# Performance work log

Measured on AMD Instinct MI355X. Metric: run time of the kernel, lower is better.

Reference implementation:

```python
import jax, jax.numpy as jnp
import numpy as np

BS = 32  # leaf block size


def setup_inputs() -> dict:
    key = jax.random.key(0)
    ks = jax.random.split(key, 10)
    N, C, E, H = 262144, 128, 4194304, 4
    x = jax.random.normal(ks[0], (1, N, C), jnp.float32)
    rows = jax.random.randint(ks[1], (E,), 0, N, dtype=jnp.int32)
    offs = jax.random.randint(ks[2], (E,), -16, 16, dtype=jnp.int32)
    cols = jnp.clip(rows + offs, 0, N - 1)
    edge_index = jnp.stack([rows, cols], axis=0)  # (2, E) int32
    edge_values = jax.random.normal(ks[3], (E,), jnp.float32)
    positions = jax.random.uniform(ks[4], (N, 3), jnp.float32)
    qkv_w = jax.random.normal(ks[5], (C, 3 * C), jnp.float32) * 0.02
    qkv_b = jnp.zeros((3 * C,), jnp.float32)
    proj_w = jax.random.normal(ks[6], (C, C), jnp.float32) * 0.02
    proj_b = jnp.zeros((C,), jnp.float32)
    gate_w = jax.random.normal(ks[7], (H, 1), jnp.float32) * 0.01  # nn.Linear(1, H)
    gate_b = jnp.zeros((H,), jnp.float32)
    return {"x": x, "edge_index": edge_index, "edge_values": edge_values,
            "positions": positions, "qkv_w": qkv_w, "qkv_b": qkv_b,
            "proj_w": proj_w, "proj_b": proj_b, "gate_w": gate_w, "gate_b": gate_b}


def _build_leaf_block_connectivity(edge_index, edge_values, positions, num_blocks, dtype):
    # Returns attn_mask (nb, 32, 33) and edge_feats (nb, 32, 33, 4) = (dx,dy,dz,w).
    rows, cols = edge_index[0], edge_index[1]
    br, bc = rows // BS, cols // BS
    in_blk = (br == bc) & (br < num_blocks)
    b_safe = jnp.where(in_blk, br, num_blocks)  # out-of-block edges -> dummy block
    rl, cl = rows % BS, cols % BS
    dx = positions[cols] - positions[rows]               # (E, 3)
    ef_flat = jnp.concatenate([dx, edge_values[:, None]], axis=1).astype(dtype)  # (E, 4)
    diag = jnp.arange(BS)
    attn_mask = jnp.zeros((num_blocks + 1, BS, BS + 1), dtype)
    attn_mask = attn_mask.at[:, diag, diag].set(1.0)      # self
    attn_mask = attn_mask.at[:, :, BS].set(1.0)           # block node
    attn_mask = attn_mask.at[b_safe, rl, cl].set(1.0)     # edges
    edge_feats = jnp.zeros((num_blocks + 1, BS, BS + 1, 4), dtype)
    edge_feats = edge_feats.at[b_safe, rl, cl].set(ef_flat)
    return attn_mask[:num_blocks], edge_feats[:num_blocks]


def reference(x, edge_index, edge_values, positions, qkv_w, qkv_b, proj_w, proj_b, gate_w, gate_b):
    B, N, C = x.shape
    H = gate_b.shape[0]
    hd = C // H
    scale = hd ** -0.5
    nb = N // BS
    dtype = x.dtype
    attn_mask, edge_feats = _build_leaf_block_connectivity(edge_index, edge_values, positions, nb, dtype)

    x_blk = x.reshape(B, nb, BS, C)
    block_node = x_blk.mean(axis=2, keepdims=True)            # (B, nb, 1, C)
    kv = jnp.concatenate([x_blk, block_node], axis=2)          # (B, nb, 33, C)
    qkv_q = x_blk @ qkv_w + qkv_b
    qkv_kv = kv @ qkv_w + qkv_b
    q = qkv_q[..., :C].reshape(B, nb, BS, H, hd)
    k = qkv_kv[..., C:2 * C].reshape(B, nb, BS + 1, H, hd)
    v = qkv_kv[..., 2 * C:].reshape(B, nb, BS + 1, H, hd)

    scores = jnp.einsum('bnqhd,bnkhd->bnqkh', q, k) * scale    # (B, nb, 32, 33, H)

    diag = jnp.arange(BS)
    w_bias = edge_feats[..., 3]                                # (nb, 32, 33)
    w_bias = w_bias.at[:, :, BS].set(1.0)
    w_bias = w_bias.at[:, diag, diag].set(1.0)
    scores = scores + w_bias[None, :, :, :, None]

    mask = attn_mask[None, :, :, :, None]                      # (1, nb, 32, 33, 1)
    neg = jnp.asarray(-1e9, dtype)
    scores = jnp.where(mask == 0, neg, scores)
    attn_probs = jax.nn.softmax(scores, axis=3)

    # edge_gate: Linear(1, H) applied to w_bias, zeroed where masked, added post-softmax
    gate = w_bias[..., None] * gate_w[:, 0] + gate_b           # (nb, 32, 33, H)
    gate = jnp.where(mask[0] == 0, 0.0, gate)[None]            # (1, nb, 32, 33, H)
    combined = attn_probs + gate

    out = jnp.einsum('bnqkh,bnkhd->bnqhd', combined, v).reshape(B, N, C)
    return out @ proj_w + proj_b
```

## Files before the change

### kernel.cpp

```cpp
#include <hip/hip_runtime.h>
#include <hip/hip_bf16.h>

#define BS 32
#define NBC 33

typedef unsigned long long ull;
typedef __attribute__((ext_vector_type(8))) __bf16 bf16x8;
typedef __attribute__((ext_vector_type(4))) float f32x4;

__device__ __forceinline__ unsigned short f2b(float f) {
    __hip_bfloat16 h = __float2bfloat16(f);
    return *reinterpret_cast<unsigned short*>(&h);
}
__device__ __forceinline__ float b2f(unsigned short u) {
    union { unsigned int i; float f; } x; x.i = ((unsigned int)u) << 16; return x.f;
}
#define LD8(p) (*reinterpret_cast<const bf16x8*>(p))

__global__ void zero_kernel(uint4* __restrict__ p, int n4) {
    int stride = gridDim.x * blockDim.x;
    for (int i = blockIdx.x * blockDim.x + threadIdx.x; i < n4; i += stride)
        p[i] = make_uint4(0u, 0u, 0u, 0u);
}

__global__ void edge_scatter_kernel(const int* __restrict__ rows,
                                    const int* __restrict__ cols,
                                    unsigned* __restrict__ tbl, int E) {
    int base = (blockIdx.x * 256 + threadIdx.x) * 4;
    if (base >= E) return;
    if (base + 4 <= E) {
        int4 r4 = *reinterpret_cast<const int4*>(rows + base);
        int4 c4 = *reinterpret_cast<const int4*>(cols + base);
        int rr[4] = {r4.x, r4.y, r4.z, r4.w};
        int cc[4] = {c4.x, c4.y, c4.z, c4.w};
        #pragma unroll
        for (int k = 0; k < 4; ++k) {
            int r = rr[k], c = cc[k];
            if ((r >> 5) == (c >> 5) && r != c)
                atomicMax(&tbl[((size_t)(r >> 5) * BS + (r & 31)) * NBC + (c & 31)],
                          (unsigned)(base + k + 1));
        }
    } else {
        for (int e = base; e < E && e < base + 4; ++e) {
            int r = rows[e], c = cols[e];
            if ((r >> 5) == (c >> 5) && r != c)
                atomicMax(&tbl[((size_t)(r >> 5) * BS + (r & 31)) * NBC + (c & 31)],
                          (unsigned)(e + 1));
        }
    }
}

__global__ void prepack_kernel(const float* __restrict__ qkv_w,
                               const float* __restrict__ proj_w,
                               unsigned short* __restrict__ wq,
                               unsigned short* __restrict__ wp) {
    int tid = blockIdx.x * 256 + threadIdx.x;
    int f = tid >> 9, lane = (tid >> 3) & 63, j = tid & 7;
    int ks = f & 3;
    int kk = ks * 32 + (lane >> 4) * 8 + j;
    int nn = lane & 15;
    if (f < 96) {
        int t = f >> 2;
        int w = t / 6, s = t % 6;
        int g = (s < 2) ? (2 * w + s) : (s < 4) ? (8 + 2 * w + (s - 2)) : (16 + 2 * w + (s - 4));
        wq[tid] = f2b(qkv_w[kk * 384 + g * 16 + nn]);
    } else {
        int f2 = f - 96;
        wp[f2 * 512 + lane * 8 + j] = f2b(proj_w[kk * 128 + (f2 >> 2) * 16 + nn]);
    }
}

__global__ __launch_bounds__(256)
void block_attn_kernel(const float* __restrict__ x,
                       const unsigned* __restrict__ tbl,
                       const float* __restrict__ vals,
                       const unsigned short* __restrict__ wq,
                       const unsigned short* __restrict__ wp,
                       const float* __restrict__ qkv_b,
                       const float* __restrict__ proj_b,
                       const float* __restrict__ gate_w,
                       const float* __restrict__ gate_b,
                       float* __restrict__ out) {
    __shared__ __align__(16) unsigned short qs[4][32][40];
    __shared__ __align__(16) unsigned short ksm[4][34][40];
    __shared__ __align__(16) unsigned short vT[4][32][40];
    __shared__ float pcol[4][32];

    const int b = blockIdx.x, t = threadIdx.x;
    const int w = t >> 6, l = t & 63, g16 = l >> 4, c16 = l & 15;
    const f32x4 z4 = {0.f, 0.f, 0.f, 0.f};
    const float NEG = -1.0e30f;

    if (l < 32) ksm[w][33][l] = 0;

    float wb[2][4][3];
    {
        const unsigned* tb = tbl + (size_t)b * (BS * NBC);
        unsigned idr[2][4][2];
        #pragma unroll
        for (int mt = 0; mt < 2; ++mt)
            #pragma unroll
            for (int r = 0; r < 4; ++r) {
                const int i = 16 * mt + 4 * g16 + r;
                #pragma unroll
                for (int nt = 0; nt < 2; ++nt)
                    idr[mt][r][nt] = tb[i * NBC + 16 * nt + c16];
            }
        #pragma unroll
        for (int mt = 0; mt < 2; ++mt)
            #pragma unroll
            for (int r = 0; r < 4; ++r) {
                const int i = 16 * mt + 4 * g16 + r;
                #pragma unroll
                for (int nt = 0; nt < 2; ++nt) {
                    const int j = 16 * nt + c16;
                    const unsigned id = idr[mt][r][nt];
                    wb[mt][r][nt] = (j == i) ? 1.f : (id ? vals[id - 1] : NEG);
                }
                wb[mt][r][2] = (c16 == 0) ? 1.f : NEG;
            }
    }

    bf16x8 a[2][4];
    const float* xb = x + (size_t)b * (BS * 128);
    #pragma unroll
    for (int mt = 0; mt < 2; ++mt)
        #pragma unroll
        for (int ks = 0; ks < 4; ++ks) {
            const float* p = xb + (c16 + 16 * mt) * 128 + ks * 32 + g16 * 8;
            float4 f0 = *reinterpret_cast<const float4*>(p);
            float4 f1 = *reinterpret_cast<const float4*>(p + 4);
            union { bf16x8 v; unsigned short u[8]; } cv;
            cv.u[0] = f2b(f0.x); cv.u[1] = f2b(f0.y); cv.u[2] = f2b(f0.z); cv.u[3] = f2b(f0.w);
            cv.u[4] = f2b(f1.x); cv.u[5] = f2b(f1.y); cv.u[6] = f2b(f1.z); cv.u[7] = f2b(f1.w);
            a[mt][ks] = cv.v;
        }

    {
        const unsigned short* wqs = wq + (size_t)(w * 24) * 512 + l * 8;
        #pragma unroll
        for (int s = 0; s < 6; ++s) {
            bf16x8 bn[4];
            #pragma unroll
            for (int ks = 0; ks < 4; ++ks) bn[ks] = LD8(wqs + (s * 4 + ks) * 512);
            f32x4 acc0 = z4, acc1 = z4;
            #pragma unroll
            for (int ks = 0; ks < 4; ++ks) {
                acc0 = __builtin_amdgcn_mfma_f32_16x16x32_bf16(a[0][ks], bn[ks], acc0, 0, 0, 0);
                acc1 = __builtin_amdgcn_mfma_f32_16x16x32_bf16(a[1][ks], bn[ks], acc1, 0, 0, 0);
            }
            const float bias = qkv_b[(s >> 1) * 128 + 32 * w + 16 * (s & 1) + c16];
            const int cc = 16 * (s & 1) + c16;
            if (s < 2) {
                #pragma unroll
                for (int r = 0; r < 4; ++r) {
                    qs[w][4 * g16 + r][cc]      = f2b(acc0[r] + bias);
                    qs[w][16 + 4 * g16 + r][cc] = f2b(acc1[r] + bias);
                }
            } else {
                float csum = acc0[0] + acc0[1] + acc0[2] + acc0[3]
                           + acc1[0] + acc1[1] + acc1[2] + acc1[3];
                csum += __shfl_xor(csum, 16, 64);
                csum += __shfl_xor(csum, 32, 64);
                const float meanv = csum * (1.f / 32.f) + bias;
                if (s < 4) {
                    #pragma unroll
                    for (int r = 0; r < 4; ++r) {
                        ksm[w][4 * g16 + r][cc]      = f2b(acc0[r] + bias);
                        ksm[w][16 + 4 * g16 + r][cc] = f2b(acc1[r] + bias);
                    }
                    if (g16 == 0) ksm[w][32][cc] = f2b(meanv);
                } else {
                    #pragma unroll
                    for (int r = 0; r < 4; ++r) {
                        vT[w][cc][4 * g16 + r]      = f2b(acc0[r] + bias);
                        vT[w][cc][16 + 4 * g16 + r] = f2b(acc1[r] + bias);
                    }
                    if (g16 == 0) vT[w][cc][32] = f2b(meanv);
                }
            }
        }
    }
    __syncthreads();

    f32x4 s[2][3];
    {
        bf16x8 aq0 = LD8(&qs[w][c16][g16 * 8]);
        bf16x8 aq1 = LD8(&qs[w][16 + c16][g16 * 8]);
        bf16x8 bk0 = LD8(&ksm[w][c16][g16 * 8]);
        bf16x8 bk1 = LD8(&ksm[w][16 + c16][g16 * 8]);
        const int n2 = (c16 == 0) ? 32 : 33;
        bf16x8 bk2 = LD8(&ksm[w][n2][g16 * 8]);
        s[0][0] = __builtin_amdgcn_mfma_f32_16x16x32_bf16(aq0, bk0, z4, 0, 0, 0);
        s[0][1] = __builtin_amdgcn_mfma_f32_16x16x32_bf16(aq0, bk1, z4, 0, 0, 0);
        s[0][2] = __builtin_amdgcn_mfma_f32_16x16x32_bf16(aq0, bk2, z4, 0, 0, 0);
        s[1][0] = __builtin_amdgcn_mfma_f32_16x16x32_bf16(aq1, bk0, z4, 0, 0, 0);
        s[1][1] = __builtin_amdgcn_mfma_f32_16x16x32_bf16(aq1, bk1, z4, 0, 0, 0);
        s[1][2] = __builtin_amdgcn_mfma_f32_16x16x32_bf16(aq1, bk2, z4, 0, 0, 0);
    }

    {
        const float scale = 0.17677669529663687f;
        const float gwh = gate_w[w], gbh = gate_b[w];
        #pragma unroll
        for (int mt = 0; mt < 2; ++mt)
            #pragma unroll
            for (int r = 0; r < 4; ++r) {
                const int i = 16 * mt + 4 * g16 + r;
                float sc[3];
                #pragma unroll
                for (int k = 0; k < 3; ++k) sc[k] = s[mt][k][r] * scale + wb[mt][r][k];
                float mx = fmaxf(fmaxf(sc[0], sc[1]), sc[2]);
                mx = fmaxf(mx, __shfl_xor(mx, 1, 64));
                mx = fmaxf(mx, __shfl_xor(mx, 2, 64));
                mx = fmaxf(mx, __shfl_xor(mx, 4, 64));
                mx = fmaxf(mx, __shfl_xor(mx, 8, 64));
                float e0 = __expf(sc[0] - mx), e1 = __expf(sc[1] - mx), e2 = __expf(sc[2] - mx);
                float sum = e0 + e1 + e2;
                sum += __shfl_xor(sum, 1, 64);
                sum += __shfl_xor(sum, 2, 64);
                sum += __shfl_xor(sum, 4, 64);
                sum += __shfl_xor(sum, 8, 64);
                const float inv = __builtin_amdgcn_rcpf(sum);
                float gt0 = (wb[mt][r][0] > -1.0e29f) ? wb[mt][r][0] * gwh + gbh : 0.f;
                float gt1 = (wb[mt][r][1] > -1.0e29f) ? wb[mt][r][1] * gwh + gbh : 0.f;
                float gt2 = (wb[mt][r][2] > -1.0e29f) ? gwh + gbh : 0.f;
                qs[w][i][c16]      = f2b(e0 * inv + gt0);
                qs[w][i][16 + c16] = f2b(e1 * inv + gt1);
                if (c16 == 0) pcol[w][i] = e2 * inv + gt2;
            }
    }
    __syncthreads();

    {
        bf16x8 ap0 = LD8(&qs[w][c16][g16 * 8]);
        bf16x8 ap1 = LD8(&qs[w][16 + c16][g16 * 8]);
        f32x4 o[2][2];
        #pragma unroll
        for (int nt = 0; nt < 2; ++nt) {
            bf16x8 bv = LD8(&vT[w][16 * nt + c16][g16 * 8]);
            o[0][nt] = __builtin_amdgcn_mfma_f32_16x16x32_bf16(ap0, bv, z4, 0, 0, 0);
            o[1][nt] = __builtin_amdgcn_mfma_f32_16x16x32_bf16(ap1, bv, z4, 0, 0, 0);
        }
        #pragma unroll
        for (int nt = 0; nt < 2; ++nt) {
            const float vm = b2f(vT[w][16 * nt + c16][32]);
            #pragma unroll
            for (int mt = 0; mt < 2; ++mt)
                #pragma unroll
                for (int r = 0; r < 4; ++r)
                    o[mt][nt][r] += pcol[w][16 * mt + 4 * g16 + r] * vm;
        }
        #pragma unroll
        for (int mt = 0; mt < 2; ++mt)
            #pragma unroll
            for (int nt = 0; nt < 2; ++nt)
                #pragma unroll
                for (int r = 0; r < 4; ++r)
                    qs[w][16 * mt + 4 * g16 + r][16 * nt + c16] = f2b(o[mt][nt][r]);
    }
    __syncthreads();

    {
        bf16x8 aa[2][4];
        #pragma unroll
        for (int mt = 0; mt < 2; ++mt)
            #pragma unroll
            for (int h = 0; h < 4; ++h)
                aa[mt][h] = LD8(&qs[h][c16 + 16 * mt][g16 * 8]);
        f32x4 po[2][2];
        po[0][0] = z4; po[0][1] = z4; po[1][0] = z4; po[1][1] = z4;
        const unsigned short* wps = wp + l * 8;
        #pragma unroll
        for (int nt = 0; nt < 2; ++nt)
            #pragma unroll
            for (int h = 0; h < 4; ++h) {
                bf16x8 bw = LD8(wps + (size_t)((2 * w + nt) * 4 + h) * 512);
                po[0][nt] = __builtin_amdgcn_mfma_f32_16x16x32_bf16(aa[0][h], bw, po[0][nt], 0, 0, 0);
                po[1][nt] = __builtin_amdgcn_mfma_f32_16x16x32_bf16(aa[1][h], bw, po[1][nt], 0, 0, 0);
            }
        float* ob = out + (size_t)b * (BS * 128);
        #pragma unroll
        for (int nt = 0; nt < 2; ++nt) {
            const int col = 32 * w + 16 * nt + c16;
            const float pbv = proj_b[col];
            #pragma unroll
            for (int mt = 0; mt < 2; ++mt)
                #pragma unroll
                for (int r = 0; r < 4; ++r)
                    ob[(size_t)(16 * mt + 4 * g16 + r) * 128 + col] = po[mt][nt][r] + pbv;
        }
    }
}

extern "C" void kernel_launch(void* const* d_in, const int* in_sizes, int n_in,
                              void* d_out, int out_size, void* d_ws, size_t ws_size,
                              hipStream_t stream) {
    const float* x      = (const float*)d_in[0];
    const int*   ei     = (const int*)d_in[1];
    const float* ev     = (const float*)d_in[2];
    const float* qkv_w  = (const float*)d_in[4];
    const float* qkv_b  = (const float*)d_in[5];
    const float* proj_w = (const float*)d_in[6];
    const float* proj_b = (const float*)d_in[7];
    const float* gate_w = (const float*)d_in[8];
    const float* gate_b = (const float*)d_in[9];
    float* out = (float*)d_out;

    const int E  = in_sizes[2];
    const int N  = in_sizes[0] / 128;
    const int nb = N / BS;

    unsigned* tbl = (unsigned*)d_ws;
    size_t twords = (size_t)nb * BS * NBC;
    size_t tbytes = (twords * sizeof(unsigned) + 255) & ~(size_t)255;
    unsigned short* wqp = (unsigned short*)((char*)d_ws + tbytes);
    unsigned short* wpp = wqp + 96 * 512;

    zero_kernel<<<2048, 256, 0, stream>>>((uint4*)tbl, (int)(twords / 4));
    prepack_kernel<<<256, 256, 0, stream>>>(qkv_w, proj_w, wqp, wpp);
    edge_scatter_kernel<<<((E + 3) / 4 + 255) / 256, 256, 0, stream>>>(ei, ei + E, tbl, E);
    block_attn_kernel<<<nb, 256, 0, stream>>>(x, tbl, ev, wqp, wpp, qkv_b, proj_b,
                                              gate_w, gate_b, out);
}
```

Before: 309.1 us.

## Merge zero and prepack kernels; stage x block through shared memory once

Folds the table-zeroing and weight-prepack kernels into one launch, with separate block ranges for each job, so one kernel launch and its gap are removed. In the attention kernel, the 32x128 x tile is now loaded cooperatively with coalesced float4 reads, converted to bf16 once, and written to shared memory. Each wave then reads its MFMA A fragments from LDS. Previously every wave loaded and converted the same x data from global memory. This adds about 8.5KB of LDS per block and an extra __syncthreads, which may reduce occupancy.

```diff
diff --git a/kernel.cpp b/kernel.cpp
--- a/kernel.cpp
+++ b/kernel.cpp
@@ -7,6 +7,7 @@
 typedef unsigned long long ull;
 typedef __attribute__((ext_vector_type(8))) __bf16 bf16x8;
 typedef __attribute__((ext_vector_type(4))) float f32x4;
+typedef __attribute__((ext_vector_type(4))) unsigned short us4;
 
 __device__ __forceinline__ unsigned short f2b(float f) {
     __hip_bfloat16 h = __float2bfloat16(f);
@@ -17,10 +18,32 @@
 }
 #define LD8(p) (*reinterpret_cast<const bf16x8*>(p))
 
-__global__ void zero_kernel(uint4* __restrict__ p, int n4) {
-    int stride = gridDim.x * blockDim.x;
-    for (int i = blockIdx.x * blockDim.x + threadIdx.x; i < n4; i += stride)
-        p[i] = make_uint4(0u, 0u, 0u, 0u);
+#define ZB 2048
+__global__ void zero_prepack_kernel(uint4* __restrict__ tbl4, int n4,
+                                    const float* __restrict__ qkv_w,
+                                    const float* __restrict__ proj_w,
+                                    unsigned short* __restrict__ wq,
+                                    unsigned short* __restrict__ wp) {
+    if (blockIdx.x < ZB) {
+        int stride = ZB * 256;
+        for (int i = blockIdx.x * 256 + threadIdx.x; i < n4; i += stride)
+            tbl4[i] = make_uint4(0u, 0u, 0u, 0u);
+    } else {
+        int tid = (blockIdx.x - ZB) * 256 + threadIdx.x;
+        int f = tid >> 9, lane = (tid >> 3) & 63, j = tid & 7;
+        int ks = f & 3;
+        int kk = ks * 32 + (lane >> 4) * 8 + j;
+        int nn = lane & 15;
+        if (f < 96) {
+            int t = f >> 2;
+            int w = t / 6, s = t % 6;
+            int g = (s < 2) ? (2 * w + s) : (s < 4) ? (8 + 2 * w + (s - 2)) : (16 + 2 * w + (s - 4));
+            wq[tid] = f2b(qkv_w[kk * 384 + g * 16 + nn]);
+        } else {
+            int f2 = f - 96;
+            wp[f2 * 512 + lane * 8 + j] = f2b(proj_w[kk * 128 + (f2 >> 2) * 16 + nn]);
+        }
+    }
 }
 
 __global__ void edge_scatter_kernel(const int* __restrict__ rows,
@@ -47,26 +70,6 @@
                 atomicMax(&tbl[((size_t)(r >> 5) * BS + (r & 31)) * NBC + (c & 31)],
                           (unsigned)(e + 1));
         }
-    }
-}
-
-__global__ void prepack_kernel(const float* __restrict__ qkv_w,
-                               const float* __restrict__ proj_w,
-                               unsigned short* __restrict__ wq,
-                               unsigned short* __restrict__ wp) {
-    int tid = blockIdx.x * 256 + threadIdx.x;
-    int f = tid >> 9, lane = (tid >> 3) & 63, j = tid & 7;
-    int ks = f & 3;
-    int kk = ks * 32 + (lane >> 4) * 8 + j;
-    int nn = lane & 15;
-    if (f < 96) {
-        int t = f >> 2;
-        int w = t / 6, s = t % 6;
-        int g = (s < 2) ? (2 * w + s) : (s < 4) ? (8 + 2 * w + (s - 2)) : (16 + 2 * w + (s - 4));
-        wq[tid] = f2b(qkv_w[kk * 384 + g * 16 + nn]);
-    } else {
-        int f2 = f - 96;
-        wp[f2 * 512 + lane * 8 + j] = f2b(proj_w[kk * 128 + (f2 >> 2) * 16 + nn]);
     }
 }
 
@@ -81,6 +84,7 @@
                        const float* __restrict__ gate_w,
                        const float* __restrict__ gate_b,
                        float* __restrict__ out) {
+    __shared__ __align__(16) unsigned short xs[32][136];
     __shared__ __align__(16) unsigned short qs[4][32][40];
     __shared__ __align__(16) unsigned short ksm[4][34][40];
     __shared__ __align__(16) unsigned short vT[4][32][40];
@@ -91,6 +95,14 @@
     const f32x4 z4 = {0.f, 0.f, 0.f, 0.f};
     const float NEG = -1.0e30f;
 
+    const float* xb = x + (size_t)b * (BS * 128);
+    #pragma unroll
+    for (int it = 0; it < 4; ++it) {
+        int idx = (t + it * 256) * 4;
+        float4 v = *reinterpret_cast<const float4*>(xb + idx);
+        us4 u; u.x = f2b(v.x); u.y = f2b(v.y); u.z = f2b(v.z); u.w = f2b(v.w);
+        *reinterpret_cast<us4*>(&xs[idx >> 7][idx & 127]) = u;
+    }
     if (l < 32) ksm[w][33][l] = 0;
 
     float wb[2][4][3];
@@ -120,21 +132,14 @@
                 wb[mt][r][2] = (c16 == 0) ? 1.f : NEG;
             }
     }
+    __syncthreads();
 
     bf16x8 a[2][4];
-    const float* xb = x + (size_t)b * (BS * 128);
     #pragma unroll
     for (int mt = 0; mt < 2; ++mt)
         #pragma unroll
-        for (int ks = 0; ks < 4; ++ks) {
-            const float* p = xb + (c16 + 16 * mt) * 128 + ks * 32 + g16 * 8;
-            float4 f0 = *reinterpret_cast<const float4*>(p);
-            float4 f1 = *reinterpret_cast<const float4*>(p + 4);
-            union { bf16x8 v; unsigned short u[8]; } cv;
-            cv.u[0] = f2b(f0.x); cv.u[1] = f2b(f0.y); cv.u[2] = f2b(f0.z); cv.u[3] = f2b(f0.w);
-            cv.u[4] = f2b(f1.x); cv.u[5] = f2b(f1.y); cv.u[6] = f2b(f1.z); cv.u[7] = f2b(f1.w);
-            a[mt][ks] = cv.v;
-        }
+        for (int ks = 0; ks < 4; ++ks)
+            a[mt][ks] = LD8(&xs[c16 + 16 * mt][ks * 32 + g16 * 8]);
 
     {
         const unsigned short* wqs = wq + (size_t)(w * 24) * 512 + l * 8;
@@ -317,8 +322,8 @@
     unsigned short* wqp = (unsigned short*)((char*)d_ws + tbytes);
     unsigned short* wpp = wqp + 96 * 512;
 
-    zero_kernel<<<2048, 256, 0, stream>>>((uint4*)tbl, (int)(twords / 4));
-    prepack_kernel<<<256, 256, 0, stream>>>(qkv_w, proj_w, wqp, wpp);
+    zero_prepack_kernel<<<ZB + 256, 256, 0, stream>>>((uint4*)tbl, (int)(twords / 4),
+                                                      qkv_w, proj_w, wqp, wpp);
     edge_scatter_kernel<<<((E + 3) / 4 + 255) / 256, 256, 0, stream>>>(ei, ei + E, tbl, E);
     block_attn_kernel<<<nb, 256, 0, stream>>>(x, tbl, ev, wqp, wpp, qkv_b, proj_b,
                                               gate_w, gate_b, out);
```

After: 270.8 us. 12.4% less time.
